# Kernel tuning notes

Hardware: AMD Instinct MI355X
Metric: run time of the kernel (lower is better)

Reference implementation:

```python
import jax, jax.numpy as jnp
import numpy as np

N_NODES = 100000
N_EDGES = 1000000
EMB_DIM = 64
N_LAYERS = 5
NUM_CLASS = 10
NUM_GRAPHS = 128
BN_EPS = 1e-5


def setup_inputs() -> dict:
    key = jax.random.key(0)
    ks = jax.random.split(key, 16)
    s = 0.05
    inp = {
        "x": jnp.zeros((N_NODES,), dtype=jnp.int64),
        "edge_index": jax.random.randint(ks[0], (2, N_EDGES), 0, N_NODES, dtype=jnp.int64),
        "edge_attr": jax.random.normal(ks[1], (N_EDGES, 7), dtype=jnp.float32),
        "batch": jnp.sort(jax.random.randint(ks[2], (N_NODES,), 0, NUM_GRAPHS, dtype=jnp.int64)),
        # parameters
        "node_table": jax.random.normal(ks[3], (1, EMB_DIM), dtype=jnp.float32) * s,
        "ew": jax.random.normal(ks[4], (N_LAYERS, 7, EMB_DIM), dtype=jnp.float32) * s,   # edge_encoder weight
        "eb": jax.random.normal(ks[5], (N_LAYERS, EMB_DIM), dtype=jnp.float32) * s,
        "w1": jax.random.normal(ks[6], (N_LAYERS, EMB_DIM, EMB_DIM), dtype=jnp.float32) * s,
        "b1": jax.random.normal(ks[7], (N_LAYERS, EMB_DIM), dtype=jnp.float32) * s,
        "w2": jax.random.normal(ks[8], (N_LAYERS, EMB_DIM, EMB_DIM), dtype=jnp.float32) * s,
        "b2": jax.random.normal(ks[9], (N_LAYERS, EMB_DIM), dtype=jnp.float32) * s,
        "gamma": jnp.ones((N_LAYERS, EMB_DIM), dtype=jnp.float32),
        "beta": jnp.zeros((N_LAYERS, EMB_DIM), dtype=jnp.float32),
        "pw": jax.random.normal(ks[10], (EMB_DIM, NUM_CLASS), dtype=jnp.float32) * s,
        "pb": jnp.zeros((NUM_CLASS,), dtype=jnp.float32),
    }
    return inp


def reference(x, edge_index, edge_attr, batch, node_table, ew, eb, w1, b1, w2, b2, gamma, beta, pw, pb):
    n = x.shape[0]
    src, dst = edge_index[0], edge_index[1]
    h = node_table[x]  # [N, D] node embedding lookup (all index 0)
    for l in range(N_LAYERS):
        edge_emb = edge_attr @ ew[l] + eb[l]                      # [E, D]
        msg = jax.nn.relu(h[src] + edge_emb)                      # gather + add + relu
        agg = jax.ops.segment_sum(msg, dst, num_segments=n)       # scatter-add
        z = h + agg                                               # (1 + eps)*x with eps=0
        z = jax.nn.relu(z @ w1[l] + b1[l]) @ w2[l] + b2[l]        # GIN MLP
        mu = z.mean(axis=0)
        var = z.var(axis=0)                                       # biased var, matches BN training
        z = (z - mu) * jax.lax.rsqrt(var + BN_EPS) * gamma[l] + beta[l]
        if l != N_LAYERS - 1:
            z = jax.nn.relu(z)                                    # dropout is identity (eval)
        h = z
    # global mean pool over graphs
    sums = jax.ops.segment_sum(h, batch, num_segments=NUM_GRAPHS)           # [B, D]
    cnt = jax.ops.segment_sum(jnp.ones((n,), h.dtype), batch, num_segments=NUM_GRAPHS)
    h_graph = sums / jnp.maximum(cnt, 1.0)[:, None]
    return h_graph @ pw + pb
```

## Files before the change

kernel.cpp:

```cpp
#include <hip/hip_runtime.h>


__global__ void hist_k(const int* __restrict__ dst, int* __restrict__ cnt, int E) {
  int stride = gridDim.x * blockDim.x;
  for (int i = blockIdx.x * blockDim.x + threadIdx.x; i < E; i += stride)
    atomicAdd(&cnt[dst[i]], 1);
}

__global__ void scan_a_k(const int* __restrict__ deg, int* __restrict__ rowptr,
                         int* __restrict__ bsum, int n) {
  __shared__ int s[256];
  int i = blockIdx.x * 256 + threadIdx.x;
  int v = (i < n) ? deg[i] : 0;
  s[threadIdx.x] = v;
  __syncthreads();
  for (int off = 1; off < 256; off <<= 1) {
    int t = (threadIdx.x >= off) ? s[threadIdx.x - off] : 0;
    __syncthreads();
    s[threadIdx.x] += t;
    __syncthreads();
  }
  if (i < n) rowptr[i] = s[threadIdx.x] - v;
  if (threadIdx.x == 255) bsum[blockIdx.x] = s[255];
}

__global__ void scan_b_k(int* __restrict__ bsum, int nb) {
  __shared__ int s[512];
  int t = threadIdx.x;
  int v = (t < nb) ? bsum[t] : 0;
  s[t] = v;
  __syncthreads();
  for (int off = 1; off < 512; off <<= 1) {
    int u = (t >= off) ? s[t - off] : 0;
    __syncthreads();
    s[t] += u;
    __syncthreads();
  }
  if (t < nb) bsum[t] = s[t] - v;
}

__global__ void scan_c_k(int* __restrict__ rowptr, int* __restrict__ cur,
                         const int* __restrict__ bsum, int n, int E) {
  int i = blockIdx.x * 256 + threadIdx.x;
  if (i < n) {
    int r = rowptr[i] + bsum[blockIdx.x];
    rowptr[i] = r;
    cur[i] = r;
  }
  if (i == 0) rowptr[n] = E;
}

__global__ void scatter_k(const int* __restrict__ src, const int* __restrict__ dst,
                          int* __restrict__ cur, float* __restrict__ sea,
                          const float* __restrict__ ea, int E) {
  int stride = gridDim.x * blockDim.x;
  for (int i = blockIdx.x * blockDim.x + threadIdx.x; i < E; i += stride) {
    int d = dst[i];
    int pos = atomicAdd(&cur[d], 1);
    const float* a = ea + (size_t)i * 7;
    float4 lo = make_float4(a[0], a[1], a[2], a[3]);
    float4 hi = make_float4(a[4], a[5], a[6], __int_as_float(src[i]));
    float4* o = (float4*)(sea + (size_t)pos * 8);
    o[0] = lo;
    o[1] = hi;
  }
}

#define NPW 8
template<int MODE>
__global__ __launch_bounds__(256)
void agg_k(const float* __restrict__ hprev, const int* __restrict__ x,
           const float* __restrict__ ntab, const int* __restrict__ rowptr,
           const float* __restrict__ sea, const float* __restrict__ ewl,
           const float* __restrict__ ebl, const float* __restrict__ stats,
           const float* __restrict__ gam, const float* __restrict__ bet,
           float* __restrict__ zout, int n) {
  int wv = (blockIdx.x * blockDim.x + threadIdx.x) >> 6;
  int lane = threadIdx.x & 63;
  int g0 = wv * NPW;
  if (g0 >= n) return;
  int gend = g0 + NPW; if (gend > n) gend = n;

  float ew_[7];
#pragma unroll
  for (int k = 0; k < 7; k++) ew_[k] = ewl[k * 64 + lane];
  float ebv = ebl[lane];

  float cnst = 0.f, sc = 1.f, sh = 0.f;
  if (MODE == 0) cnst = ntab[lane];
  if (MODE == 2) {
    float s1 = stats[lane], s2 = stats[64 + lane];
    float mu = s1 / (float)n;
    float var = s2 / (float)n - mu * mu;
    sc = gam[lane] * rsqrtf(var + 1e-5f);
    sh = bet[lane] - mu * sc;
  }

  auto Hg = [&](int row) -> float {
    if (MODE == 1) {
      int xv = __builtin_amdgcn_readfirstlane(x[row]);
      return ntab[(size_t)xv * 64 + lane];
    } else {
      float v = hprev[(size_t)row * 64 + lane];
      return fmaxf(fmaf(v, sc, sh), 0.f);
    }
  };

  int pcur = __builtin_amdgcn_readfirstlane(rowptr[g0]);
  for (int nd = g0; nd < gend; nd++) {
    int pnext = __builtin_amdgcn_readfirstlane(rowptr[nd + 1]);
    float acc;
    if (MODE == 0) acc = cnst;
    else acc = Hg(nd);
    int p = pcur;
    for (; p + 4 <= pnext; p += 4) {
      const float* R0 = sea + (size_t)p * 8;
      const float* R1 = R0 + 8;
      const float* R2 = R0 + 16;
      const float* R3 = R0 + 24;
      float h0 = 0.f, h1 = 0.f, h2 = 0.f, h3 = 0.f;
      if (MODE != 0) {
        int s0 = __builtin_amdgcn_readfirstlane(__float_as_int(R0[7]));
        int s1 = __builtin_amdgcn_readfirstlane(__float_as_int(R1[7]));
        int s2 = __builtin_amdgcn_readfirstlane(__float_as_int(R2[7]));
        int s3 = __builtin_amdgcn_readfirstlane(__float_as_int(R3[7]));
        h0 = Hg(s0); h1 = Hg(s1); h2 = Hg(s2); h3 = Hg(s3);
      } else {
        h0 = h1 = h2 = h3 = cnst;
      }
      float m0 = ebv, m1 = ebv, m2 = ebv, m3 = ebv;
#pragma unroll
      for (int k = 0; k < 7; k++) {
        m0 = fmaf(R0[k], ew_[k], m0);
        m1 = fmaf(R1[k], ew_[k], m1);
        m2 = fmaf(R2[k], ew_[k], m2);
        m3 = fmaf(R3[k], ew_[k], m3);
      }
      acc += fmaxf(h0 + m0, 0.f);
      acc += fmaxf(h1 + m1, 0.f);
      acc += fmaxf(h2 + m2, 0.f);
      acc += fmaxf(h3 + m3, 0.f);
    }
    for (; p < pnext; p++) {
      const float* R0 = sea + (size_t)p * 8;
      float h0 = cnst;
      if (MODE != 0) {
        int s0 = __builtin_amdgcn_readfirstlane(__float_as_int(R0[7]));
        h0 = Hg(s0);
      }
      float m0 = ebv;
#pragma unroll
      for (int k = 0; k < 7; k++) m0 = fmaf(R0[k], ew_[k], m0);
      acc += fmaxf(h0 + m0, 0.f);
    }
    zout[(size_t)nd * 64 + lane] = acc;
    pcur = pnext;
  }
}

#define ASTR 132
__global__ __launch_bounds__(256, 3)
void mlp_k(const float* __restrict__ zin, const float* __restrict__ w1l,
           const float* __restrict__ b1l, const float* __restrict__ w2l,
           const float* __restrict__ b2l, float* __restrict__ zout,
           float* __restrict__ statslot, int n) {
  __shared__ float As[64 * ASTR];
  __shared__ float Ws[4096];
  __shared__ float red[128];
  int tid = threadIdx.x;
  int tx = tid & 15, ty = tid >> 4;
  if (tid < 128) red[tid] = 0.f;
  int r0 = blockIdx.x * 128;

  {
    const float4* gz = (const float4*)(zin + (size_t)r0 * 64);
#pragma unroll
    for (int it = 0; it < 8; it++) {
      int f4 = it * 256 + tid;
      int row = f4 >> 4, kq = f4 & 15;
      float4 v = make_float4(0.f, 0.f, 0.f, 0.f);
      if (r0 + row < n) v = gz[f4];
      As[(4 * kq + 0) * ASTR + row] = v.x;
      As[(4 * kq + 1) * ASTR + row] = v.y;
      As[(4 * kq + 2) * ASTR + row] = v.z;
      As[(4 * kq + 3) * ASTR + row] = v.w;
    }
    const float4* wa = (const float4*)w1l;
    float4* wd = (float4*)Ws;
#pragma unroll
    for (int it = 0; it < 4; it++) wd[it * 256 + tid] = wa[it * 256 + tid];
  }
  __syncthreads();

  const float4 b1v = *(const float4*)(b1l + tx * 4);
  float t[8][4];
#pragma unroll
  for (int rr = 0; rr < 8; rr++) {
    t[rr][0] = b1v.x; t[rr][1] = b1v.y; t[rr][2] = b1v.z; t[rr][3] = b1v.w;
  }
#pragma unroll 8
  for (int k = 0; k < 64; k++) {
    float4 aA = *(const float4*)&As[k * ASTR + ty * 8];
    float4 aB = *(const float4*)&As[k * ASTR + ty * 8 + 4];
    float4 b = *(const float4*)&Ws[k * 64 + tx * 4];
    float a[8] = {aA.x, aA.y, aA.z, aA.w, aB.x, aB.y, aB.z, aB.w};
#pragma unroll
    for (int rr = 0; rr < 8; rr++) {
      t[rr][0] = fmaf(a[rr], b.x, t[rr][0]);
      t[rr][1] = fmaf(a[rr], b.y, t[rr][1]);
      t[rr][2] = fmaf(a[rr], b.z, t[rr][2]);
      t[rr][3] = fmaf(a[rr], b.w, t[rr][3]);
    }
  }
  __syncthreads();

#pragma unroll
  for (int cc = 0; cc < 4; cc++)
#pragma unroll
    for (int rr = 0; rr < 8; rr++)
      As[(tx * 4 + cc) * ASTR + ty * 8 + rr] = fmaxf(t[rr][cc], 0.f);
  {
    const float4* wb = (const float4*)w2l;
    float4* wd = (float4*)Ws;
#pragma unroll
    for (int it = 0; it < 4; it++) wd[it * 256 + tid] = wb[it * 256 + tid];
  }
  __syncthreads();

  const float4 b2v = *(const float4*)(b2l + tx * 4);
  float o[8][4];
#pragma unroll
  for (int rr = 0; rr < 8; rr++) {
    o[rr][0] = b2v.x; o[rr][1] = b2v.y; o[rr][2] = b2v.z; o[rr][3] = b2v.w;
  }
#pragma unroll 8
  for (int k = 0; k < 64; k++) {
    float4 aA = *(const float4*)&As[k * ASTR + ty * 8];
    float4 aB = *(const float4*)&As[k * ASTR + ty * 8 + 4];
    float4 b = *(const float4*)&Ws[k * 64 + tx * 4];
    float a[8] = {aA.x, aA.y, aA.z, aA.w, aB.x, aB.y, aB.z, aB.w};
#pragma unroll
    for (int rr = 0; rr < 8; rr++) {
      o[rr][0] = fmaf(a[rr], b.x, o[rr][0]);
      o[rr][1] = fmaf(a[rr], b.y, o[rr][1]);
      o[rr][2] = fmaf(a[rr], b.z, o[rr][2]);
      o[rr][3] = fmaf(a[rr], b.w, o[rr][3]);
    }
  }

  float s1[4] = {0.f, 0.f, 0.f, 0.f}, s2[4] = {0.f, 0.f, 0.f, 0.f};
#pragma unroll
  for (int rr = 0; rr < 8; rr++) {
    int grow = r0 + ty * 8 + rr;
    if (grow < n) {
      float4 v = make_float4(o[rr][0], o[rr][1], o[rr][2], o[rr][3]);
      *(float4*)(zout + (size_t)grow * 64 + tx * 4) = v;
#pragma unroll
      for (int cc = 0; cc < 4; cc++) {
        s1[cc] += o[rr][cc];
        s2[cc] = fmaf(o[rr][cc], o[rr][cc], s2[cc]);
      }
    }
  }
#pragma unroll
  for (int cc = 0; cc < 4; cc++) {
    s1[cc] += __shfl_xor(s1[cc], 16); s1[cc] += __shfl_xor(s1[cc], 32);
    s2[cc] += __shfl_xor(s2[cc], 16); s2[cc] += __shfl_xor(s2[cc], 32);
  }
  if ((tid & 48) == 0) {
#pragma unroll
    for (int cc = 0; cc < 4; cc++) {
      atomicAdd(&red[tx * 4 + cc], s1[cc]);
      atomicAdd(&red[64 + tx * 4 + cc], s2[cc]);
    }
  }
  __syncthreads();
  if (tid < 128) atomicAdd(&statslot[tid], red[tid]);
}

__global__ void pool_k(const float* __restrict__ z2, const float* __restrict__ stats,
                       const float* __restrict__ gam, const float* __restrict__ bet,
                       const int* __restrict__ batch, float* __restrict__ gsum,
                       float* __restrict__ gcnt, int n, int ch) {
  int wid = (blockIdx.x * blockDim.x + threadIdx.x) >> 6;
  int lane = threadIdx.x & 63;
  int v0 = wid * ch;
  if (v0 >= n) return;
  int v1 = v0 + ch; if (v1 > n) v1 = n;
  float st1 = stats[lane], st2 = stats[64 + lane];
  float mu = st1 / (float)n;
  float var = st2 / (float)n - mu * mu;
  float sc = gam[lane] * rsqrtf(var + 1e-5f);
  float sh = bet[lane] - mu * sc;
  int curb = batch[v0];
  float acc = 0.f;
  int cnt = 0;
  for (int v = v0; v < v1; v++) {
    int b = batch[v];
    if (b != curb) {
      atomicAdd(&gsum[curb * 64 + lane], acc);
      if (lane == 0) atomicAdd(&gcnt[curb], (float)cnt);
      acc = 0.f; cnt = 0; curb = b;
    }
    acc += fmaf(z2[(size_t)v * 64 + lane], sc, sh);
    cnt++;
  }
  atomicAdd(&gsum[curb * 64 + lane], acc);
  if (lane == 0) atomicAdd(&gcnt[curb], (float)cnt);
}

__global__ void head_k(const float* __restrict__ gsum, const float* __restrict__ gcnt,
                       const float* __restrict__ pw, const float* __restrict__ pb,
                       float* __restrict__ out, int B, int C) {
  for (int idx = threadIdx.x; idx < B * C; idx += blockDim.x) {
    int g = idx / C, c = idx % C;
    float inv = 1.f / fmaxf(gcnt[g], 1.f);
    float s = pb[c];
    for (int d = 0; d < 64; d++)
      s = fmaf(gsum[g * 64 + d] * inv, pw[d * C + c], s);
    out[idx] = s;
  }
}

extern "C" void kernel_launch(void* const* d_in, const int* in_sizes, int n_in,
                              void* d_out, int out_size, void* d_ws, size_t ws_size,
                              hipStream_t stream) {
  const int*   x     = (const int*)d_in[0];
  const int*   ei    = (const int*)d_in[1];
  const float* ea    = (const float*)d_in[2];
  const int*   batch = (const int*)d_in[3];
  const float* ntab  = (const float*)d_in[4];
  const float* ew    = (const float*)d_in[5];
  const float* eb    = (const float*)d_in[6];
  const float* w1    = (const float*)d_in[7];
  const float* b1    = (const float*)d_in[8];
  const float* w2    = (const float*)d_in[9];
  const float* b2    = (const float*)d_in[10];
  const float* gamma = (const float*)d_in[11];
  const float* beta  = (const float*)d_in[12];
  const float* pw    = (const float*)d_in[13];
  const float* pb    = (const float*)d_in[14];
  float* out = (float*)d_out;

  int N = in_sizes[0];
  int E = in_sizes[1] / 2;
  int L = in_sizes[6] / 64;
  int C = in_sizes[14];
  int B = out_size / C;
  bool tab1 = (in_sizes[4] == 64);

  const int* src = ei;
  const int* dst = ei + E;

  char* ws = (char*)d_ws;
  auto alloc = [&](size_t bytes) -> char* {
    char* p = ws;
    ws += (bytes + 255) & ~(size_t)255;
    return p;
  };
  float* zA      = (float*)alloc((size_t)N * 64 * 4);
  float* zB      = (float*)alloc((size_t)N * 64 * 4);
  int*   rowptr  = (int*)alloc((size_t)(N + 1) * 4);
  int*   cur     = (int*)alloc((size_t)N * 4);
  float* sea     = (float*)alloc((size_t)E * 8 * 4);
  int*   bsum    = (int*)alloc(512 * 4);
  float* bnstats = (float*)alloc((size_t)L * 128 * 4);
  float* gsum    = (float*)alloc((size_t)B * 64 * 4);
  float* gcnt    = (float*)alloc((size_t)B * 4);

  hipMemsetAsync(cur, 0, (size_t)N * 4, stream);
  hipMemsetAsync(bnstats, 0, (size_t)L * 128 * 4, stream);
  hipMemsetAsync(gsum, 0, (size_t)B * 64 * 4, stream);
  hipMemsetAsync(gcnt, 0, (size_t)B * 4, stream);

  hist_k<<<2048, 256, 0, stream>>>(dst, cur, E);
  int NB = (N + 255) / 256;
  scan_a_k<<<NB, 256, 0, stream>>>(cur, rowptr, bsum, N);
  scan_b_k<<<1, 512, 0, stream>>>(bsum, NB);
  scan_c_k<<<NB, 256, 0, stream>>>(rowptr, cur, bsum, N, E);
  scatter_k<<<4096, 256, 0, stream>>>(src, dst, cur, sea, ea, E);

  int aggWaves = (N + NPW - 1) / NPW;
  int aggBlocks = (aggWaves * 64 + 255) / 256;
  int mlpBlocks = (N + 127) / 128;
  for (int l = 0; l < L; l++) {
    const float* ewl = ew + (size_t)l * 448;
    const float* ebl = eb + (size_t)l * 64;
    const float* stP = bnstats + (size_t)(l > 0 ? l - 1 : 0) * 128;
    const float* gmP = gamma + (size_t)(l > 0 ? l - 1 : 0) * 64;
    const float* btP = beta + (size_t)(l > 0 ? l - 1 : 0) * 64;
    if (l == 0) {
      if (tab1)
        agg_k<0><<<aggBlocks, 256, 0, stream>>>(zB, x, ntab, rowptr, sea, ewl, ebl,
                                                stP, gmP, btP, zA, N);
      else
        agg_k<1><<<aggBlocks, 256, 0, stream>>>(zB, x, ntab, rowptr, sea, ewl, ebl,
                                                stP, gmP, btP, zA, N);
    } else {
      agg_k<2><<<aggBlocks, 256, 0, stream>>>(zB, x, ntab, rowptr, sea, ewl, ebl,
                                              stP, gmP, btP, zA, N);
    }
    mlp_k<<<mlpBlocks, 256, 0, stream>>>(zA, w1 + (size_t)l * 4096, b1 + (size_t)l * 64,
                                         w2 + (size_t)l * 4096, b2 + (size_t)l * 64,
                                         zB, bnstats + (size_t)l * 128, N);
  }

  int ch = 128;
  int poolWaves = (N + ch - 1) / ch;
  int poolBlocks = (poolWaves + 3) / 4;
  pool_k<<<poolBlocks, 256, 0, stream>>>(zB, bnstats + (size_t)(L - 1) * 128,
                                         gamma + (size_t)(L - 1) * 64,
                                         beta + (size_t)(L - 1) * 64,
                                         batch, gsum, gcnt, N, ch);
  head_k<<<1, 256, 0, stream>>>(gsum, gcnt, pw, pb, out, B, C);
}
```

Baseline: 654.1 us.

## Fuse edge aggregation into GIN MLP kernel via shared-memory tile

Merges the per-layer aggregation kernel and the MLP kernel into one. Each 256-thread block aggregates 128 nodes (32 per wave) and writes the sums straight into the shared-memory A tile, so the N×64 intermediate never goes to global memory and one launch per layer is saved. Layer outputs now ping-pong between two buffers. The cost is less aggregation parallelism: 32 nodes per wave instead of 8, under a launch bound of 3 blocks per SM and a large LDS footprint, so the latency-bound gathers may hide less well.

```diff
diff --git a/kernel.cpp b/kernel.cpp
--- a/kernel.cpp
+++ b/kernel.cpp
@@ -66,34 +66,45 @@
   }
 }
 
-#define NPW 8
+#define ASTR 132
 template<int MODE>
-__global__ __launch_bounds__(256)
-void agg_k(const float* __restrict__ hprev, const int* __restrict__ x,
-           const float* __restrict__ ntab, const int* __restrict__ rowptr,
-           const float* __restrict__ sea, const float* __restrict__ ewl,
-           const float* __restrict__ ebl, const float* __restrict__ stats,
-           const float* __restrict__ gam, const float* __restrict__ bet,
-           float* __restrict__ zout, int n) {
-  int wv = (blockIdx.x * blockDim.x + threadIdx.x) >> 6;
-  int lane = threadIdx.x & 63;
-  int g0 = wv * NPW;
-  if (g0 >= n) return;
-  int gend = g0 + NPW; if (gend > n) gend = n;
+__global__ __launch_bounds__(256, 3)
+void fused_k(const float* __restrict__ hprev, const int* __restrict__ x,
+             const float* __restrict__ ntab, const int* __restrict__ rowptr,
+             const float* __restrict__ sea, const float* __restrict__ ewl,
+             const float* __restrict__ ebl, const float* __restrict__ statsP,
+             const float* __restrict__ gamP, const float* __restrict__ betP,
+             const float* __restrict__ w1l, const float* __restrict__ b1l,
+             const float* __restrict__ w2l, const float* __restrict__ b2l,
+             float* __restrict__ zout, float* __restrict__ statslot, int n) {
+  __shared__ float As[64 * ASTR];
+  __shared__ float Ws[4096];
+  __shared__ float red[128];
+  int tid = threadIdx.x;
+  int lane = tid & 63, wv = tid >> 6;
+  int tx = tid & 15, ty = tid >> 4;
+  if (tid < 128) red[tid] = 0.f;
+  int r0 = blockIdx.x * 128;
+
+  {
+    const float4* wa = (const float4*)w1l;
+    float4* wd = (float4*)Ws;
+#pragma unroll
+    for (int it = 0; it < 4; it++) wd[it * 256 + tid] = wa[it * 256 + tid];
+  }
 
   float ew_[7];
 #pragma unroll
   for (int k = 0; k < 7; k++) ew_[k] = ewl[k * 64 + lane];
   float ebv = ebl[lane];
-
   float cnst = 0.f, sc = 1.f, sh = 0.f;
   if (MODE == 0) cnst = ntab[lane];
   if (MODE == 2) {
-    float s1 = stats[lane], s2 = stats[64 + lane];
+    float s1 = statsP[lane], s2 = statsP[64 + lane];
     float mu = s1 / (float)n;
     float var = s2 / (float)n - mu * mu;
-    sc = gam[lane] * rsqrtf(var + 1e-5f);
-    sh = bet[lane] - mu * sc;
+    sc = gamP[lane] * rsqrtf(var + 1e-5f);
+    sh = betP[lane] - mu * sc;
   }
 
   auto Hg = [&](int row) -> float {
@@ -106,90 +117,60 @@
     }
   };
 
-  int pcur = __builtin_amdgcn_readfirstlane(rowptr[g0]);
-  for (int nd = g0; nd < gend; nd++) {
-    int pnext = __builtin_amdgcn_readfirstlane(rowptr[nd + 1]);
-    float acc;
-    if (MODE == 0) acc = cnst;
-    else acc = Hg(nd);
-    int p = pcur;
-    for (; p + 4 <= pnext; p += 4) {
-      const float* R0 = sea + (size_t)p * 8;
-      const float* R1 = R0 + 8;
-      const float* R2 = R0 + 16;
-      const float* R3 = R0 + 24;
-      float h0 = 0.f, h1 = 0.f, h2 = 0.f, h3 = 0.f;
-      if (MODE != 0) {
-        int s0 = __builtin_amdgcn_readfirstlane(__float_as_int(R0[7]));
-        int s1 = __builtin_amdgcn_readfirstlane(__float_as_int(R1[7]));
-        int s2 = __builtin_amdgcn_readfirstlane(__float_as_int(R2[7]));
-        int s3 = __builtin_amdgcn_readfirstlane(__float_as_int(R3[7]));
-        h0 = Hg(s0); h1 = Hg(s1); h2 = Hg(s2); h3 = Hg(s3);
-      } else {
-        h0 = h1 = h2 = h3 = cnst;
+  int g0 = r0 + wv * 32;
+  int gend = g0 + 32; if (gend > n) gend = n;
+  if (g0 < n) {
+    int pcur = __builtin_amdgcn_readfirstlane(rowptr[g0]);
+    for (int nd = g0; nd < gend; nd++) {
+      int pnext = __builtin_amdgcn_readfirstlane(rowptr[nd + 1]);
+      float acc = (MODE == 0) ? cnst : Hg(nd);
+      int p = pcur;
+      for (; p + 4 <= pnext; p += 4) {
+        const float* R0 = sea + (size_t)p * 8;
+        const float* R1 = R0 + 8;
+        const float* R2 = R0 + 16;
+        const float* R3 = R0 + 24;
+        float h0, h1, h2, h3;
+        if (MODE != 0) {
+          int s0 = __builtin_amdgcn_readfirstlane(__float_as_int(R0[7]));
+          int s1 = __builtin_amdgcn_readfirstlane(__float_as_int(R1[7]));
+          int s2 = __builtin_amdgcn_readfirstlane(__float_as_int(R2[7]));
+          int s3 = __builtin_amdgcn_readfirstlane(__float_as_int(R3[7]));
+          h0 = Hg(s0); h1 = Hg(s1); h2 = Hg(s2); h3 = Hg(s3);
+        } else {
+          h0 = h1 = h2 = h3 = cnst;
+        }
+        float m0 = ebv, m1 = ebv, m2 = ebv, m3 = ebv;
+#pragma unroll
+        for (int k = 0; k < 7; k++) {
+          m0 = fmaf(R0[k], ew_[k], m0);
+          m1 = fmaf(R1[k], ew_[k], m1);
+          m2 = fmaf(R2[k], ew_[k], m2);
+          m3 = fmaf(R3[k], ew_[k], m3);
+        }
+        acc += fmaxf(h0 + m0, 0.f);
+        acc += fmaxf(h1 + m1, 0.f);
+        acc += fmaxf(h2 + m2, 0.f);
+        acc += fmaxf(h3 + m3, 0.f);
       }
-      float m0 = ebv, m1 = ebv, m2 = ebv, m3 = ebv;
-#pragma unroll
-      for (int k = 0; k < 7; k++) {
-        m0 = fmaf(R0[k], ew_[k], m0);
-        m1 = fmaf(R1[k], ew_[k], m1);
-        m2 = fmaf(R2[k], ew_[k], m2);
-        m3 = fmaf(R3[k], ew_[k], m3);
+      for (; p < pnext; p++) {
+        const float* R0 = sea + (size_t)p * 8;
+        float h0 = cnst;
+        if (MODE != 0) {
+          int s0 = __builtin_amdgcn_readfirstlane(__float_as_int(R0[7]));
+          h0 = Hg(s0);
+        }
+        float m0 = ebv;
+#pragma unroll
+        for (int k = 0; k < 7; k++) m0 = fmaf(R0[k], ew_[k], m0);
+        acc += fmaxf(h0 + m0, 0.f);
       }
-      acc += fmaxf(h0 + m0, 0.f);
-      acc += fmaxf(h1 + m1, 0.f);
-      acc += fmaxf(h2 + m2, 0.f);
-      acc += fmaxf(h3 + m3, 0.f);
-    }
-    for (; p < pnext; p++) {
-      const float* R0 = sea + (size_t)p * 8;
-      float h0 = cnst;
-      if (MODE != 0) {
-        int s0 = __builtin_amdgcn_readfirstlane(__float_as_int(R0[7]));
-        h0 = Hg(s0);
-      }
-      float m0 = ebv;
-#pragma unroll
-      for (int k = 0; k < 7; k++) m0 = fmaf(R0[k], ew_[k], m0);
-      acc += fmaxf(h0 + m0, 0.f);
-    }
-    zout[(size_t)nd * 64 + lane] = acc;
-    pcur = pnext;
-  }
-}
-
-#define ASTR 132
-__global__ __launch_bounds__(256, 3)
-void mlp_k(const float* __restrict__ zin, const float* __restrict__ w1l,
-           const float* __restrict__ b1l, const float* __restrict__ w2l,
-           const float* __restrict__ b2l, float* __restrict__ zout,
-           float* __restrict__ statslot, int n) {
-  __shared__ float As[64 * ASTR];
-  __shared__ float Ws[4096];
-  __shared__ float red[128];
-  int tid = threadIdx.x;
-  int tx = tid & 15, ty = tid >> 4;
-  if (tid < 128) red[tid] = 0.f;
-  int r0 = blockIdx.x * 128;
-
-  {
-    const float4* gz = (const float4*)(zin + (size_t)r0 * 64);
-#pragma unroll
-    for (int it = 0; it < 8; it++) {
-      int f4 = it * 256 + tid;
-      int row = f4 >> 4, kq = f4 & 15;
-      float4 v = make_float4(0.f, 0.f, 0.f, 0.f);
-      if (r0 + row < n) v = gz[f4];
-      As[(4 * kq + 0) * ASTR + row] = v.x;
-      As[(4 * kq + 1) * ASTR + row] = v.y;
-      As[(4 * kq + 2) * ASTR + row] = v.z;
-      As[(4 * kq + 3) * ASTR + row] = v.w;
-    }
-    const float4* wa = (const float4*)w1l;
-    float4* wd = (float4*)Ws;
-#pragma unroll
-    for (int it = 0; it < 4; it++) wd[it * 256 + tid] = wa[it * 256 + tid];
-  }
+      As[lane * ASTR + (nd - r0)] = acc;
+      pcur = pnext;
+    }
+  }
+  for (int nd = (g0 < n ? gend : g0); nd < g0 + 32; nd++)
+    As[lane * ASTR + (nd - r0)] = 0.f;
   __syncthreads();
 
   const float4 b1v = *(const float4*)(b1l + tx * 4);
@@ -358,8 +339,8 @@
     ws += (bytes + 255) & ~(size_t)255;
     return p;
   };
-  float* zA      = (float*)alloc((size_t)N * 64 * 4);
-  float* zB      = (float*)alloc((size_t)N * 64 * 4);
+  float* z0      = (float*)alloc((size_t)N * 64 * 4);
+  float* z1      = (float*)alloc((size_t)N * 64 * 4);
   int*   rowptr  = (int*)alloc((size_t)(N + 1) * 4);
   int*   cur     = (int*)alloc((size_t)N * 4);
   float* sea     = (float*)alloc((size_t)E * 8 * 4);
@@ -367,6 +348,7 @@
   float* bnstats = (float*)alloc((size_t)L * 128 * 4);
   float* gsum    = (float*)alloc((size_t)B * 64 * 4);
   float* gcnt    = (float*)alloc((size_t)B * 4);
+  float* zbuf[2] = {z0, z1};
 
   hipMemsetAsync(cur, 0, (size_t)N * 4, stream);
   hipMemsetAsync(bnstats, 0, (size_t)L * 128 * 4, stream);
@@ -380,35 +362,41 @@
   scan_c_k<<<NB, 256, 0, stream>>>(rowptr, cur, bsum, N, E);
   scatter_k<<<4096, 256, 0, stream>>>(src, dst, cur, sea, ea, E);
 
-  int aggWaves = (N + NPW - 1) / NPW;
-  int aggBlocks = (aggWaves * 64 + 255) / 256;
-  int mlpBlocks = (N + 127) / 128;
+  int blocks = (N + 127) / 128;
   for (int l = 0; l < L; l++) {
     const float* ewl = ew + (size_t)l * 448;
     const float* ebl = eb + (size_t)l * 64;
+    const float* hprev = zbuf[(l + 1) & 1];
+    float*       zcur  = zbuf[l & 1];
     const float* stP = bnstats + (size_t)(l > 0 ? l - 1 : 0) * 128;
     const float* gmP = gamma + (size_t)(l > 0 ? l - 1 : 0) * 64;
     const float* btP = beta + (size_t)(l > 0 ? l - 1 : 0) * 64;
+    const float* w1l = w1 + (size_t)l * 4096;
+    const float* b1l = b1 + (size_t)l * 64;
+    const float* w2l = w2 + (size_t)l * 4096;
+    const float* b2l = b2 + (size_t)l * 64;
+    float* slot = bnstats + (size_t)l * 128;
     if (l == 0) {
       if (tab1)
-        agg_k<0><<<aggBlocks, 256, 0, stream>>>(zB, x, ntab, rowptr, sea, ewl, ebl,
-                                                stP, gmP, btP, zA, N);
+        fused_k<0><<<blocks, 256, 0, stream>>>(hprev, x, ntab, rowptr, sea, ewl, ebl,
+                                               stP, gmP, btP, w1l, b1l, w2l, b2l,
+                                               zcur, slot, N);
       else
-        agg_k<1><<<aggBlocks, 256, 0, stream>>>(zB, x, ntab, rowptr, sea, ewl, ebl,
-                                                stP, gmP, btP, zA, N);
+        fused_k<1><<<blocks, 256, 0, stream>>>(hprev, x, ntab, rowptr, sea, ewl, ebl,
+                                               stP, gmP, btP, w1l, b1l, w2l, b2l,
+                                               zcur, slot, N);
     } else {
-      agg_k<2><<<aggBlocks, 256, 0, stream>>>(zB, x, ntab, rowptr, sea, ewl, ebl,
-                                              stP, gmP, btP, zA, N);
-    }
-    mlp_k<<<mlpBlocks, 256, 0, stream>>>(zA, w1 + (size_t)l * 4096, b1 + (size_t)l * 64,
-                                         w2 + (size_t)l * 4096, b2 + (size_t)l * 64,
-                                         zB, bnstats + (size_t)l * 128, N);
+      fused_k<2><<<blocks, 256, 0, stream>>>(hprev, x, ntab, rowptr, sea, ewl, ebl,
+                                             stP, gmP, btP, w1l, b1l, w2l, b2l,
+                                             zcur, slot, N);
+    }
   }
 
   int ch = 128;
   int poolWaves = (N + ch - 1) / ch;
   int poolBlocks = (poolWaves + 3) / 4;
-  pool_k<<<poolBlocks, 256, 0, stream>>>(zB, bnstats + (size_t)(L - 1) * 128,
+  pool_k<<<poolBlocks, 256, 0, stream>>>(zbuf[(L - 1) & 1],
+                                         bnstats + (size_t)(L - 1) * 128,
                                          gamma + (size_t)(L - 1) * 64,
                                          beta + (size_t)(L - 1) * 64,
                                          batch, gsum, gcnt, N, ch);
```

After: 991.8 us. 1.52x slower.

## Software-pipeline edge loads in aggregation kernel across node boundaries

Applied to the files above, without the earlier changes.

The aggregation kernel's per-node edge loop becomes a flat loop over the wave's whole edge range. It runs in groups of four edges with double-buffered float4 loads, so the next group's edge records are issued before the current group is reduced. Node boundaries are handled inline by flushing the accumulator, which removes the per-node scalar remainder loop and the serialized readfirstlane source loads. The goal is to hide memory latency on the edge stream and the neighbor gathers. The cost is more register pressure from 16 float4 buffers and more complex control flow, and the edge buffer is padded for overread.

```diff
diff --git a/kernel.cpp b/kernel.cpp
--- a/kernel.cpp
+++ b/kernel.cpp
@@ -72,8 +72,8 @@
 void agg_k(const float* __restrict__ hprev, const int* __restrict__ x,
            const float* __restrict__ ntab, const int* __restrict__ rowptr,
            const float* __restrict__ sea, const float* __restrict__ ewl,
-           const float* __restrict__ ebl, const float* __restrict__ stats,
-           const float* __restrict__ gam, const float* __restrict__ bet,
+           const float* __restrict__ ebl, const float* __restrict__ statsP,
+           const float* __restrict__ gamP, const float* __restrict__ betP,
            float* __restrict__ zout, int n) {
   int wv = (blockIdx.x * blockDim.x + threadIdx.x) >> 6;
   int lane = threadIdx.x & 63;
@@ -89,73 +89,103 @@
   float cnst = 0.f, sc = 1.f, sh = 0.f;
   if (MODE == 0) cnst = ntab[lane];
   if (MODE == 2) {
-    float s1 = stats[lane], s2 = stats[64 + lane];
+    float s1 = statsP[lane], s2 = statsP[64 + lane];
     float mu = s1 / (float)n;
     float var = s2 / (float)n - mu * mu;
-    sc = gam[lane] * rsqrtf(var + 1e-5f);
-    sh = bet[lane] - mu * sc;
-  }
-
-  auto Hg = [&](int row) -> float {
-    if (MODE == 1) {
-      int xv = __builtin_amdgcn_readfirstlane(x[row]);
-      return ntab[(size_t)xv * 64 + lane];
-    } else {
-      float v = hprev[(size_t)row * 64 + lane];
-      return fmaxf(fmaf(v, sc, sh), 0.f);
-    }
+    sc = gamP[lane] * rsqrtf(var + 1e-5f);
+    sh = betP[lane] - mu * sc;
+  }
+
+  auto self_ld = [&](int nd) -> float {
+    if (MODE == 0) return 0.f;
+    if (MODE == 1) { int xv = x[nd]; return ntab[(size_t)xv * 64 + lane]; }
+    return hprev[(size_t)nd * 64 + lane];
   };
-
-  int pcur = __builtin_amdgcn_readfirstlane(rowptr[g0]);
-  for (int nd = g0; nd < gend; nd++) {
-    int pnext = __builtin_amdgcn_readfirstlane(rowptr[nd + 1]);
-    float acc;
-    if (MODE == 0) acc = cnst;
-    else acc = Hg(nd);
-    int p = pcur;
-    for (; p + 4 <= pnext; p += 4) {
-      const float* R0 = sea + (size_t)p * 8;
-      const float* R1 = R0 + 8;
-      const float* R2 = R0 + 16;
-      const float* R3 = R0 + 24;
-      float h0 = 0.f, h1 = 0.f, h2 = 0.f, h3 = 0.f;
-      if (MODE != 0) {
-        int s0 = __builtin_amdgcn_readfirstlane(__float_as_int(R0[7]));
-        int s1 = __builtin_amdgcn_readfirstlane(__float_as_int(R1[7]));
-        int s2 = __builtin_amdgcn_readfirstlane(__float_as_int(R2[7]));
-        int s3 = __builtin_amdgcn_readfirstlane(__float_as_int(R3[7]));
-        h0 = Hg(s0); h1 = Hg(s1); h2 = Hg(s2); h3 = Hg(s3);
-      } else {
-        h0 = h1 = h2 = h3 = cnst;
+  auto finish_h = [&](float v) -> float {
+    if (MODE == 0) return cnst;
+    if (MODE == 1) return v;
+    return fmaxf(fmaf(v, sc, sh), 0.f);
+  };
+
+  int P1 = __builtin_amdgcn_readfirstlane(rowptr[gend]);
+  int p  = __builtin_amdgcn_readfirstlane(rowptr[g0]);
+  int nd = g0;
+  int pn = __builtin_amdgcn_readfirstlane(rowptr[nd + 1]);
+  float selfv = self_ld(nd);
+  float acc = 0.f;
+
+  float4 la0, la1, la2, la3, ha0, ha1, ha2, ha3;
+  float4 lb0, lb1, lb2, lb3, hb0, hb1, hb2, hb3;
+
+#define ISSUE(L0, L1, L2, L3, H0, H1, H2, H3, PP)                              \
+  {                                                                            \
+    int pv_;                                                                   \
+    asm volatile("v_mov_b32 %0, %1" : "=v"(pv_) : "s"(PP));                    \
+    const float4* bp_ = (const float4*)sea + (size_t)(unsigned)pv_ * 2;       \
+    L0 = bp_[0]; H0 = bp_[1]; L1 = bp_[2]; H1 = bp_[3];                        \
+    L2 = bp_[4]; H2 = bp_[5]; L3 = bp_[6]; H3 = bp_[7];                        \
+  }
+
+#define GATH1(HIU, HGU, PE)                                                    \
+  float HGU = 0.f;                                                             \
+  if (MODE != 0) {                                                             \
+    int s_ = __float_as_int(HIU.w);                                            \
+    if ((PE) >= P1) s_ = 0;                                                    \
+    if (MODE == 1) { int xv_ = x[s_]; HGU = ntab[(size_t)xv_ * 64 + lane]; }   \
+    else HGU = hprev[(size_t)s_ * 64 + lane];                                  \
+  }
+
+#define FIN1(LOU, HIU, HGU, PE)                                                \
+  if ((PE) < P1) {                                                             \
+    while ((PE) >= pn) {                                                       \
+      zout[(size_t)nd * 64 + lane] = finish_h(selfv) + acc;                    \
+      nd++;                                                                    \
+      selfv = self_ld(nd);                                                     \
+      pn = __builtin_amdgcn_readfirstlane(rowptr[nd + 1]);                     \
+      acc = 0.f;                                                               \
+    }                                                                          \
+    float m_ = ebv;                                                            \
+    m_ = fmaf(LOU.x, ew_[0], m_); m_ = fmaf(LOU.y, ew_[1], m_);                \
+    m_ = fmaf(LOU.z, ew_[2], m_); m_ = fmaf(LOU.w, ew_[3], m_);                \
+    m_ = fmaf(HIU.x, ew_[4], m_); m_ = fmaf(HIU.y, ew_[5], m_);                \
+    m_ = fmaf(HIU.z, ew_[6], m_);                                              \
+    float h_ = finish_h(HGU);                                                  \
+    acc += fmaxf(h_ + m_, 0.f);                                                \
+  }
+
+  if (p < P1) {
+    ISSUE(la0, la1, la2, la3, ha0, ha1, ha2, ha3, p);
+    while (p < P1) {
+      {
+        GATH1(ha0, hg0, p + 0) GATH1(ha1, hg1, p + 1)
+        GATH1(ha2, hg2, p + 2) GATH1(ha3, hg3, p + 3)
+        int pb = p + 4;
+        if (pb < P1) ISSUE(lb0, lb1, lb2, lb3, hb0, hb1, hb2, hb3, pb);
+        FIN1(la0, ha0, hg0, p + 0) FIN1(la1, ha1, hg1, p + 1)
+        FIN1(la2, ha2, hg2, p + 2) FIN1(la3, ha3, hg3, p + 3)
+        p += 4;
       }
-      float m0 = ebv, m1 = ebv, m2 = ebv, m3 = ebv;
-#pragma unroll
-      for (int k = 0; k < 7; k++) {
-        m0 = fmaf(R0[k], ew_[k], m0);
-        m1 = fmaf(R1[k], ew_[k], m1);
-        m2 = fmaf(R2[k], ew_[k], m2);
-        m3 = fmaf(R3[k], ew_[k], m3);
+      if (p >= P1) break;
+      {
+        GATH1(hb0, hg0, p + 0) GATH1(hb1, hg1, p + 1)
+        GATH1(hb2, hg2, p + 2) GATH1(hb3, hg3, p + 3)
+        int pa = p + 4;
+        if (pa < P1) ISSUE(la0, la1, la2, la3, ha0, ha1, ha2, ha3, pa);
+        FIN1(lb0, hb0, hg0, p + 0) FIN1(lb1, hb1, hg1, p + 1)
+        FIN1(lb2, hb2, hg2, p + 2) FIN1(lb3, hb3, hg3, p + 3)
+        p += 4;
       }
-      acc += fmaxf(h0 + m0, 0.f);
-      acc += fmaxf(h1 + m1, 0.f);
-      acc += fmaxf(h2 + m2, 0.f);
-      acc += fmaxf(h3 + m3, 0.f);
-    }
-    for (; p < pnext; p++) {
-      const float* R0 = sea + (size_t)p * 8;
-      float h0 = cnst;
-      if (MODE != 0) {
-        int s0 = __builtin_amdgcn_readfirstlane(__float_as_int(R0[7]));
-        h0 = Hg(s0);
-      }
-      float m0 = ebv;
-#pragma unroll
-      for (int k = 0; k < 7; k++) m0 = fmaf(R0[k], ew_[k], m0);
-      acc += fmaxf(h0 + m0, 0.f);
-    }
-    zout[(size_t)nd * 64 + lane] = acc;
-    pcur = pnext;
-  }
+    }
+  }
+  while (nd < gend) {
+    zout[(size_t)nd * 64 + lane] = finish_h(selfv) + acc;
+    nd++;
+    acc = 0.f;
+    if (nd < gend) selfv = self_ld(nd);
+  }
+#undef ISSUE
+#undef GATH1
+#undef FIN1
 }
 
 #define ASTR 132
@@ -358,11 +388,11 @@
     ws += (bytes + 255) & ~(size_t)255;
     return p;
   };
-  float* zA      = (float*)alloc((size_t)N * 64 * 4);
-  float* zB      = (float*)alloc((size_t)N * 64 * 4);
+  float* hbuf    = (float*)alloc((size_t)N * 64 * 4);
+  float* tbuf    = (float*)alloc((size_t)N * 64 * 4);
   int*   rowptr  = (int*)alloc((size_t)(N + 1) * 4);
   int*   cur     = (int*)alloc((size_t)N * 4);
-  float* sea     = (float*)alloc((size_t)E * 8 * 4);
+  float* sea     = (float*)alloc((size_t)(E + 8) * 8 * 4);
   int*   bsum    = (int*)alloc(512 * 4);
   float* bnstats = (float*)alloc((size_t)L * 128 * 4);
   float* gsum    = (float*)alloc((size_t)B * 64 * 4);
@@ -391,24 +421,27 @@
     const float* btP = beta + (size_t)(l > 0 ? l - 1 : 0) * 64;
     if (l == 0) {
       if (tab1)
-        agg_k<0><<<aggBlocks, 256, 0, stream>>>(zB, x, ntab, rowptr, sea, ewl, ebl,
-                                                stP, gmP, btP, zA, N);
+        agg_k<0><<<aggBlocks, 256, 0, stream>>>(hbuf, x, ntab, rowptr, sea, ewl,
+                                                ebl, stP, gmP, btP, tbuf, N);
       else
-        agg_k<1><<<aggBlocks, 256, 0, stream>>>(zB, x, ntab, rowptr, sea, ewl, ebl,
-                                                stP, gmP, btP, zA, N);
+        agg_k<1><<<aggBlocks, 256, 0, stream>>>(hbuf, x, ntab, rowptr, sea, ewl,
+                                                ebl, stP, gmP, btP, tbuf, N);
     } else {
-      agg_k<2><<<aggBlocks, 256, 0, stream>>>(zB, x, ntab, rowptr, sea, ewl, ebl,
-                                              stP, gmP, btP, zA, N);
-    }
-    mlp_k<<<mlpBlocks, 256, 0, stream>>>(zA, w1 + (size_t)l * 4096, b1 + (size_t)l * 64,
-                                         w2 + (size_t)l * 4096, b2 + (size_t)l * 64,
-                                         zB, bnstats + (size_t)l * 128, N);
+      agg_k<2><<<aggBlocks, 256, 0, stream>>>(hbuf, x, ntab, rowptr, sea, ewl,
+                                              ebl, stP, gmP, btP, tbuf, N);
+    }
+    mlp_k<<<mlpBlocks, 256, 0, stream>>>(tbuf, w1 + (size_t)l * 4096,
+                                         b1 + (size_t)l * 64,
+                                         w2 + (size_t)l * 4096,
+                                         b2 + (size_t)l * 64,
+                                         hbuf, bnstats + (size_t)l * 128, N);
   }
 
   int ch = 128;
   int poolWaves = (N + ch - 1) / ch;
   int poolBlocks = (poolWaves + 3) / 4;
-  pool_k<<<poolBlocks, 256, 0, stream>>>(zB, bnstats + (size_t)(L - 1) * 128,
+  pool_k<<<poolBlocks, 256, 0, stream>>>(hbuf,
+                                         bnstats + (size_t)(L - 1) * 128,
                                          gamma + (size_t)(L - 1) * 64,
                                          beta + (size_t)(L - 1) * 64,
                                          batch, gsum, gcnt, N, ch);
```

After: 781.1 us. 19.4% more time.
